# Optimization experiments

Hardware: AMD Instinct MI355X
Metric: run time of the kernel (lower is better)

Reference implementation:

```python
import jax, jax.numpy as jnp
import numpy as np

B, S, D_MODEL, H = 4, 2048, 2048, 16
HD = D_MODEL // H  # 128
ROPE_BASE = 10000.0


def apply_rope(x):
    # x: [B, H, S, HD]; interleaved-pair rotary embedding along seq axis
    s, d = x.shape[2], x.shape[3]
    inv_freq = 1.0 / (ROPE_BASE ** (jnp.arange(0, d, 2, dtype=jnp.float32) / d))  # [d/2]
    ang = jnp.arange(s, dtype=jnp.float32)[:, None] * inv_freq[None, :]  # [S, d/2]
    cos, sin = jnp.cos(ang), jnp.sin(ang)
    x0, x1 = x[..., 0::2], x[..., 1::2]  # [B,H,S,d/2]
    o0 = x0 * cos - x1 * sin
    o1 = x0 * sin + x1 * cos
    return jnp.stack([o0, o1], axis=-1).reshape(x.shape)


def setup_inputs() -> dict:
    key = jax.random.key(0)
    ks = jax.random.split(key, 5)
    sc = 1.0 / np.sqrt(D_MODEL)
    return {
        "x": jax.random.normal(ks[0], (B, S, D_MODEL), dtype=jnp.float32),
        "Wq": jax.random.normal(ks[1], (D_MODEL, D_MODEL), dtype=jnp.float32) * sc,
        "Wk": jax.random.normal(ks[2], (D_MODEL, D_MODEL), dtype=jnp.float32) * sc,
        "Wv": jax.random.normal(ks[3], (D_MODEL, D_MODEL), dtype=jnp.float32) * sc,
        "Wo": jax.random.normal(ks[4], (D_MODEL, D_MODEL), dtype=jnp.float32) * sc,
        "bo": jnp.zeros((D_MODEL,), dtype=jnp.float32),
    }


def reference(x, Wq, Wk, Wv, Wo, bo):
    b, s, _ = x.shape
    # torch Linear: y = x @ W.T (no qkv bias)
    q = (x @ Wq.T).reshape(b, s, H, HD).transpose(0, 2, 1, 3)  # [B,H,S,HD]
    k = (x @ Wk.T).reshape(b, s, H, HD).transpose(0, 2, 1, 3)
    v = (x @ Wv.T).reshape(b, s, H, HD).transpose(0, 2, 1, 3)
    q = apply_rope(q)
    k = apply_rope(k)
    scores = jnp.einsum("bhqd,bhkd->bhqk", q, k)
    causal = jnp.tril(jnp.ones((s, s), dtype=bool))
    scores = jnp.where(causal, scores, -jnp.inf)
    attn = jax.nn.softmax(scores / jnp.sqrt(jnp.float32(HD)), axis=-1)
    # dropout p=0.0 -> identity
    ctx = jnp.einsum("bhqk,bhkd->bqhd", attn, v).reshape(b, s, H * HD)
    return ctx @ Wo.T + bo
```

## Files before the change

### kernel.cpp

```cpp
#include <hip/hip_runtime.h>
#include <hip/hip_bf16.h>
#include <math.h>

#define B_  4
#define S_  2048
#define DM  2048
#define H_  16
#define HD_ 128

typedef __bf16 bf16;
typedef __bf16 bf16x4 __attribute__((ext_vector_type(4)));
typedef __bf16 bf16x8 __attribute__((ext_vector_type(8)));
typedef float  f32x4  __attribute__((ext_vector_type(4)));

__device__ __forceinline__ void gload_lds16(const bf16* g, bf16* l) {
  __builtin_amdgcn_global_load_lds(
      (const __attribute__((address_space(1))) void*)g,
      (__attribute__((address_space(3))) void*)l, 16, 0, 0);
}

__global__ void cast_f32_bf16(const float* __restrict__ src, bf16* __restrict__ dst, int n4) {
  int stride = gridDim.x * blockDim.x;
  for (int i = blockIdx.x * blockDim.x + threadIdx.x; i < n4; i += stride) {
    float4 v = reinterpret_cast<const float4*>(src)[i];
    bf16x4 o = { (bf16)v.x, (bf16)v.y, (bf16)v.z, (bf16)v.w };
    reinterpret_cast<bf16x4*>(dst)[i] = o;
  }
}

__global__ void rope_table_k(float* __restrict__ tab) {
  int idx = blockIdx.x * blockDim.x + threadIdx.x;
  if (idx >= S_ * (HD_ / 2)) return;
  int pos = idx >> 6, i = idx & 63;
  float inv = powf(10000.0f, -(2.0f * i) / (float)HD_);
  float ang = (float)pos * inv;
  tab[2 * idx]     = cosf(ang);
  tab[2 * idx + 1] = sinf(ang);
}

template<int OUTF>
__global__ __launch_bounds__(256, 2)
void gemm_bt(const bf16* __restrict__ A, const bf16* __restrict__ Bt,
             bf16* __restrict__ Cb, float* __restrict__ Cf,
             const float* __restrict__ bias, const float* __restrict__ tab,
             float scale, int M, int N, int K) {
  __shared__ bf16 As[128][32];
  __shared__ bf16 Bs[128][32];
  const int tid = threadIdx.x;
  const int w = tid >> 6, l = tid & 63;
  const int row0 = blockIdx.x * 128, col0 = blockIdx.y * 128;
  const int wm = (w >> 1) * 64, wn = (w & 1) * 64;
  const int lr = l & 15, lg = l >> 4;
  f32x4 acc[4][4] = {};
  for (int kt = 0; kt < K; kt += 32) {
    __syncthreads();
#pragma unroll
    for (int i = 0; i < 2; ++i) {
      int eo = (i * 4096 + w * 1024) / 2 + l * 8;
      int r = eo >> 5, c = eo & 31;
      gload_lds16(A  + (size_t)(row0 + r) * K + kt + c, &As[0][0] + i * 2048 + w * 512);
      gload_lds16(Bt + (size_t)(col0 + r) * K + kt + c, &Bs[0][0] + i * 2048 + w * 512);
    }
    asm volatile("s_waitcnt vmcnt(0)" ::: "memory");
    __syncthreads();
    bf16x8 af[4], bfr[4];
#pragma unroll
    for (int mi = 0; mi < 4; ++mi)
      af[mi] = *reinterpret_cast<const bf16x8*>(&As[wm + mi * 16 + lr][lg * 8]);
#pragma unroll
    for (int ni = 0; ni < 4; ++ni)
      bfr[ni] = *reinterpret_cast<const bf16x8*>(&Bs[wn + ni * 16 + lr][lg * 8]);
#pragma unroll
    for (int mi = 0; mi < 4; ++mi)
#pragma unroll
      for (int ni = 0; ni < 4; ++ni)
        acc[mi][ni] = __builtin_amdgcn_mfma_f32_16x16x32_bf16(af[mi], bfr[ni], acc[mi][ni], 0, 0, 0);
  }
#pragma unroll
  for (int mi = 0; mi < 4; ++mi) {
    int rb = row0 + wm + mi * 16 + lg * 4;
#pragma unroll
    for (int ni = 0; ni < 4; ++ni) {
      int cc = col0 + wn + ni * 16 + lr;
      if (OUTF == 2) {
        int bb = rb >> 11, s = rb & 2047;
        int hh = cc >> 7, dd = cc & 127;
        bf16x4 pack = { (bf16)acc[mi][ni][0], (bf16)acc[mi][ni][1],
                        (bf16)acc[mi][ni][2], (bf16)acc[mi][ni][3] };
        *reinterpret_cast<bf16x4*>(Cb + (((size_t)(bb * H_ + hh) * HD_ + dd) << 11) + s) = pack;
      } else if (OUTF == 3) {
        int i2 = (cc & 127) >> 1;
        float sgn = (lr & 1) ? 1.0f : -1.0f;
#pragma unroll
        for (int j = 0; j < 4; ++j) {
          float own = acc[mi][ni][j];
          float par = __shfl_xor(own, 1);
          int s = (rb + j) & (S_ - 1);
          float2 cs = reinterpret_cast<const float2*>(tab)[s * 64 + i2];
          float outv = (own * cs.x + sgn * par * cs.y) * scale;
          Cb[(size_t)(rb + j) * N + cc] = (bf16)outv;
        }
      } else {
#pragma unroll
        for (int j = 0; j < 4; ++j) {
          size_t off = (size_t)(rb + j) * N + cc;
          if (OUTF == 1) Cf[off] = acc[mi][ni][j] + bias[cc];
          else           Cb[off] = (bf16)acc[mi][ni][j];
        }
      }
    }
  }
}

__global__ __launch_bounds__(512, 4)
void attn_fwd(const bf16* __restrict__ Q, const bf16* __restrict__ K,
              const bf16* __restrict__ Vt, bf16* __restrict__ O) {
  __shared__ bf16 Ks[2][64 * 128];
  __shared__ bf16 Vs[2][128 * 64];
  __shared__ bf16 Ps[8][16 * 64];
  const int tid = threadIdx.x;
  const int w = tid >> 6, l = tid & 63;
  const int lr = l & 15, lg = l >> 4;
  const int bx = blockIdx.x;
  const int h = blockIdx.y, b = blockIdx.z;
  const size_t bbase = (size_t)b * S_ * DM + (size_t)h * HD_;
  const bf16* vtb = Vt + (size_t)(b * H_ + h) * HD_ * S_;

#pragma unroll 1
  for (int pass = 0; pass < 2; ++pass) {
    const int qt = pass ? bx : (15 - bx);
    const int q0 = qt * 128 + w * 16;
    const int ktmax = 2 * qt + 1;

    bf16x8 qf[4];
#pragma unroll
    for (int kb = 0; kb < 4; ++kb)
      qf[kb] = *reinterpret_cast<const bf16x8*>(Q + bbase + (size_t)(q0 + lr) * DM + kb * 32 + lg * 8);

    float m_r = -INFINITY;
    float l_r = 0.f;
    f32x4 o[8] = {};

#pragma unroll
    for (int i = 0; i < 2; ++i) {
      int X = w * 2048 + i * 1024 + l * 16;
      int r = X >> 8, scb = (X & 255) ^ ((r & 7) << 4);
      gload_lds16(K + bbase + (size_t)r * DM + (scb >> 1), &Ks[0][(w * 2048 + i * 1024) >> 1]);
    }
#pragma unroll
    for (int i = 0; i < 2; ++i) {
      int X = w * 2048 + i * 1024 + l * 16;
      int d = X >> 7, scb = (X & 127) ^ ((d & 7) << 4);
      gload_lds16(vtb + (size_t)d * S_ + (scb >> 1), &Vs[0][(w * 2048 + i * 1024) >> 1]);
    }

    for (int kt = 0; kt <= ktmax; ++kt) {
      const int buf = kt & 1;
      if (kt < ktmax) {
        const int nk = (kt + 1) * 64;
#pragma unroll
        for (int i = 0; i < 2; ++i) {
          int X = w * 2048 + i * 1024 + l * 16;
          int r = X >> 8, scb = (X & 255) ^ ((r & 7) << 4);
          gload_lds16(K + bbase + (size_t)(nk + r) * DM + (scb >> 1),
                      &Ks[buf ^ 1][(w * 2048 + i * 1024) >> 1]);
        }
#pragma unroll
        for (int i = 0; i < 2; ++i) {
          int X = w * 2048 + i * 1024 + l * 16;
          int d = X >> 7, scb = (X & 127) ^ ((d & 7) << 4);
          gload_lds16(vtb + (size_t)d * S_ + nk + (scb >> 1),
                      &Vs[buf ^ 1][(w * 2048 + i * 1024) >> 1]);
        }
        asm volatile("s_waitcnt vmcnt(4)" ::: "memory");
      } else {
        asm volatile("s_waitcnt vmcnt(0)" ::: "memory");
      }
      __builtin_amdgcn_s_barrier();

      f32x4 sc4[4];
      __builtin_amdgcn_s_setprio(1);
#pragma unroll
      for (int cb = 0; cb < 4; ++cb) {
        sc4[cb] = f32x4{0.f, 0.f, 0.f, 0.f};
        int r = cb * 16 + lr;
#pragma unroll
        for (int kb = 0; kb < 4; ++kb) {
          int off = r * 256 + ((kb * 64 + lg * 16) ^ ((lr & 7) << 4));
          bf16x8 kf = *reinterpret_cast<const bf16x8*>((const char*)Ks[buf] + off);
          sc4[cb] = __builtin_amdgcn_mfma_f32_16x16x32_bf16(kf, qf[kb], sc4[cb], 0, 0, 0);
        }
      }
      __builtin_amdgcn_s_setprio(0);

      const int kv0 = kt * 64;
      if (kv0 + 63 > q0) {
        const int qq = q0 + lr;
#pragma unroll
        for (int cb = 0; cb < 4; ++cb)
#pragma unroll
          for (int jj = 0; jj < 4; ++jj)
            if (kv0 + cb * 16 + lg * 4 + jj > qq) sc4[cb][jj] = -INFINITY;
      }

      float tm = -INFINITY;
#pragma unroll
      for (int cb = 0; cb < 4; ++cb)
#pragma unroll
        for (int jj = 0; jj < 4; ++jj) tm = fmaxf(tm, sc4[cb][jj]);
      tm = fmaxf(tm, __shfl_xor(tm, 16));
      tm = fmaxf(tm, __shfl_xor(tm, 32));
      float mnew = fmaxf(m_r, tm);
      float sc_f = __expf(m_r - mnew);
      m_r = mnew;
      float rs = 0.f;
#pragma unroll
      for (int cb = 0; cb < 4; ++cb)
#pragma unroll
        for (int jj = 0; jj < 4; ++jj) {
          float p = __expf(sc4[cb][jj] - mnew);
          sc4[cb][jj] = p;
          rs += p;
        }
      rs += __shfl_xor(rs, 16);
      rs += __shfl_xor(rs, 32);
      l_r = l_r * sc_f + rs;

      float scO[4];
#pragma unroll
      for (int j = 0; j < 4; ++j) scO[j] = __shfl(sc_f, lg * 4 + j);
#pragma unroll
      for (int nb = 0; nb < 8; ++nb)
#pragma unroll
        for (int j = 0; j < 4; ++j) o[nb][j] *= scO[j];

#pragma unroll
      for (int cb = 0; cb < 4; ++cb) {
        bf16x4 pk = { (bf16)sc4[cb][0], (bf16)sc4[cb][1], (bf16)sc4[cb][2], (bf16)sc4[cb][3] };
        int off = lr * 128 + ((cb * 32 + lg * 8) ^ ((lr & 7) << 4));
        *reinterpret_cast<bf16x4*>((char*)Ps[w] + off) = pk;
      }

      bf16x8 pf[2];
#pragma unroll
      for (int kc = 0; kc < 2; ++kc) {
        int off = lr * 128 + ((kc * 64 + lg * 16) ^ ((lr & 7) << 4));
        pf[kc] = *reinterpret_cast<const bf16x8*>((const char*)Ps[w] + off);
      }
      __builtin_amdgcn_s_setprio(1);
#pragma unroll
      for (int nb = 0; nb < 8; ++nb) {
        int d = nb * 16 + lr;
#pragma unroll
        for (int kc = 0; kc < 2; ++kc) {
          int off = d * 128 + ((kc * 64 + lg * 16) ^ ((lr & 7) << 4));
          bf16x8 vf = *reinterpret_cast<const bf16x8*>((const char*)Vs[buf] + off);
          o[nb] = __builtin_amdgcn_mfma_f32_16x16x32_bf16(pf[kc], vf, o[nb], 0, 0, 0);
        }
      }
      __builtin_amdgcn_s_setprio(0);

      asm volatile("s_waitcnt lgkmcnt(0)" ::: "memory");
      __builtin_amdgcn_s_barrier();
    }

    float lO[4];
#pragma unroll
    for (int j = 0; j < 4; ++j) lO[j] = __shfl(l_r, lg * 4 + j);
#pragma unroll
    for (int j = 0; j < 4; ++j) {
      float inv = 1.0f / lO[j];
      size_t rowoff = bbase + (size_t)(q0 + lg * 4 + j) * DM;
#pragma unroll
      for (int nb = 0; nb < 8; ++nb)
        O[rowoff + nb * 16 + lr] = (bf16)(o[nb][j] * inv);
    }
  }
}

extern "C" void kernel_launch(void* const* d_in, const int* in_sizes, int n_in,
                              void* d_out, int out_size, void* d_ws, size_t ws_size,
                              hipStream_t stream) {
  const float* x  = (const float*)d_in[0];
  const float* Wq = (const float*)d_in[1];
  const float* Wk = (const float*)d_in[2];
  const float* Wv = (const float*)d_in[3];
  const float* Wo = (const float*)d_in[4];
  const float* bo = (const float*)d_in[5];
  float* out = (float*)d_out;

  const size_t NX = (size_t)B_ * S_ * DM;
  const size_t NW = (size_t)DM * DM;
  char* ws = (char*)d_ws;
  bf16* xb   = (bf16*)ws; ws += NX * 2;
  bf16* wqb  = (bf16*)ws; ws += NW * 2;
  bf16* wkb  = (bf16*)ws; ws += NW * 2;
  bf16* wvb  = (bf16*)ws; ws += NW * 2;
  bf16* wob  = (bf16*)ws; ws += NW * 2;
  bf16* qb   = (bf16*)ws; ws += NX * 2;
  bf16* kb   = (bf16*)ws; ws += NX * 2;
  bf16* vt   = (bf16*)ws; ws += NX * 2;
  bf16* ctxb = (bf16*)ws; ws += NX * 2;
  float* tab = (float*)ws; ws += (size_t)S_ * 64 * 2 * sizeof(float);

  cast_f32_bf16<<<(int)((NX / 4 + 255) / 256), 256, 0, stream>>>(x, xb, (int)(NX / 4));
  cast_f32_bf16<<<(int)((NW / 4 + 255) / 256), 256, 0, stream>>>(Wq, wqb, (int)(NW / 4));
  cast_f32_bf16<<<(int)((NW / 4 + 255) / 256), 256, 0, stream>>>(Wk, wkb, (int)(NW / 4));
  cast_f32_bf16<<<(int)((NW / 4 + 255) / 256), 256, 0, stream>>>(Wv, wvb, (int)(NW / 4));
  cast_f32_bf16<<<(int)((NW / 4 + 255) / 256), 256, 0, stream>>>(Wo, wob, (int)(NW / 4));
  rope_table_k<<<(S_ * 64 + 255) / 256, 256, 0, stream>>>(tab);

  const int M = B_ * S_;
  dim3 gg(M / 128, DM / 128);
  gemm_bt<3><<<gg, 256, 0, stream>>>(xb, wqb, qb, nullptr, nullptr, tab, 0.08838834764831845f, M, DM, DM);
  gemm_bt<3><<<gg, 256, 0, stream>>>(xb, wkb, kb, nullptr, nullptr, tab, 1.0f, M, DM, DM);
  gemm_bt<2><<<gg, 256, 0, stream>>>(xb, wvb, vt, nullptr, nullptr, nullptr, 0.f, M, DM, DM);

  attn_fwd<<<dim3(8, H_, B_), 512, 0, stream>>>(qb, kb, vt, ctxb);

  gemm_bt<1><<<gg, 256, 0, stream>>>(ctxb, wob, nullptr, out, bo, nullptr, 0.f, M, DM, DM);
}
```

Baseline: 487.1 us.

## Fuse QKV projections into one 512x128-tile GEMM with triple-buffered swizzled LDS

Replaces the 128x128 single-buffered GEMM with a 512-thread kernel that computes 512x128 tiles. Global-to-LDS loads run through a three-stage ring buffer with partial vmcnt waits, and the LDS layout is XOR-swizzled to avoid bank conflicts. The Q, K and V weights are concatenated so a single launch produces all three projections, with the epilogue choosing RoPE or the transposed V store by column region. The aim is more operand reuse per tile, loads overlapped with MFMA work, and fewer launches. The cost is higher register and LDS use (about 120KB LDS), which lowers occupancy.

```diff
diff --git a/kernel.cpp b/kernel.cpp
--- a/kernel.cpp
+++ b/kernel.cpp
@@ -38,74 +38,116 @@
   tab[2 * idx + 1] = sinf(ang);
 }
 
-template<int OUTF>
-__global__ __launch_bounds__(256, 2)
-void gemm_bt(const bf16* __restrict__ A, const bf16* __restrict__ Bt,
-             bf16* __restrict__ Cb, float* __restrict__ Cf,
-             const float* __restrict__ bias, const float* __restrict__ tab,
-             float scale, int M, int N, int K) {
-  __shared__ bf16 As[128][32];
-  __shared__ bf16 Bs[128][32];
+template<int EPI>
+__global__ __launch_bounds__(512, 2)
+void gemm512(const bf16* __restrict__ A, const bf16* __restrict__ Bt,
+             bf16* __restrict__ Oq, bf16* __restrict__ Ok, bf16* __restrict__ Ovt,
+             float* __restrict__ Cf, const float* __restrict__ bias,
+             const float* __restrict__ tab, int N, int K) {
+  __shared__ bf16 lds[61440];
   const int tid = threadIdx.x;
   const int w = tid >> 6, l = tid & 63;
-  const int row0 = blockIdx.x * 128, col0 = blockIdx.y * 128;
-  const int wm = (w >> 1) * 64, wn = (w & 1) * 64;
   const int lr = l & 15, lg = l >> 4;
-  f32x4 acc[4][4] = {};
-  for (int kt = 0; kt < K; kt += 32) {
-    __syncthreads();
-#pragma unroll
-    for (int i = 0; i < 2; ++i) {
-      int eo = (i * 4096 + w * 1024) / 2 + l * 8;
-      int r = eo >> 5, c = eo & 31;
-      gload_lds16(A  + (size_t)(row0 + r) * K + kt + c, &As[0][0] + i * 2048 + w * 512);
-      gload_lds16(Bt + (size_t)(col0 + r) * K + kt + c, &Bs[0][0] + i * 2048 + w * 512);
-    }
-    asm volatile("s_waitcnt vmcnt(0)" ::: "memory");
-    __syncthreads();
-    bf16x8 af[4], bfr[4];
-#pragma unroll
-    for (int mi = 0; mi < 4; ++mi)
-      af[mi] = *reinterpret_cast<const bf16x8*>(&As[wm + mi * 16 + lr][lg * 8]);
-#pragma unroll
-    for (int ni = 0; ni < 4; ++ni)
-      bfr[ni] = *reinterpret_cast<const bf16x8*>(&Bs[wn + ni * 16 + lr][lg * 8]);
-#pragma unroll
-    for (int mi = 0; mi < 4; ++mi)
+  const int row0 = blockIdx.y * 512, col0 = blockIdx.x * 128;
+  const int wm = w >> 1, wn = w & 1;
+  const int NT = K / 32;
+
+  auto stage = [&](int t, int c) {
+    const bf16* Ab = A + (size_t)row0 * K + t * 32;
+    const bf16* Bb = Bt + (size_t)col0 * K + t * 32;
+    bf16* base = lds + c * 20480;
+#pragma unroll
+    for (int i = 0; i < 4; ++i) {
+      int D = w * 4096 + i * 1024 + l * 16;
+      int r = D >> 6;
+      int gk = ((D & 63) ^ (((r >> 1) & 3) << 4)) >> 1;
+      gload_lds16(Ab + (size_t)r * K + gk, base + ((w * 4096 + i * 1024) >> 1));
+    }
+    {
+      int D = w * 1024 + l * 16;
+      int r = D >> 6;
+      int gk = ((D & 63) ^ (((r >> 1) & 3) << 4)) >> 1;
+      gload_lds16(Bb + (size_t)r * K + gk, base + 16384 + ((w * 1024) >> 1));
+    }
+  };
+
+  int offA[8], offB[4];
+#pragma unroll
+  for (int mi = 0; mi < 8; ++mi) {
+    int r = wm * 128 + mi * 16 + lr;
+    offA[mi] = r * 64 + ((lg * 16) ^ (((r >> 1) & 3) << 4));
+  }
+#pragma unroll
+  for (int ni = 0; ni < 4; ++ni) {
+    int r = wn * 64 + ni * 16 + lr;
+    offB[ni] = 32768 + r * 64 + ((lg * 16) ^ (((r >> 1) & 3) << 4));
+  }
+
+  f32x4 acc[8][4] = {};
+  stage(0, 0);
+  stage(1, 1);
+
+  for (int t = 0; t < NT; ++t) {
+    const int c = t % 3;
+    if (t + 2 < NT) {
+      stage(t + 2, (t + 2) % 3);
+      asm volatile("s_waitcnt vmcnt(10)" ::: "memory");
+    } else if (t + 1 < NT) {
+      asm volatile("s_waitcnt vmcnt(5)" ::: "memory");
+    } else {
+      asm volatile("s_waitcnt vmcnt(0)" ::: "memory");
+    }
+    __builtin_amdgcn_s_barrier();
+
+    const char* bb = (const char*)lds + c * 40960;
+    bf16x8 af[8], bfr[4];
+#pragma unroll
+    for (int mi = 0; mi < 8; ++mi) af[mi] = *reinterpret_cast<const bf16x8*>(bb + offA[mi]);
+#pragma unroll
+    for (int ni = 0; ni < 4; ++ni) bfr[ni] = *reinterpret_cast<const bf16x8*>(bb + offB[ni]);
+
+    __builtin_amdgcn_s_setprio(1);
+#pragma unroll
+    for (int mi = 0; mi < 8; ++mi)
 #pragma unroll
       for (int ni = 0; ni < 4; ++ni)
         acc[mi][ni] = __builtin_amdgcn_mfma_f32_16x16x32_bf16(af[mi], bfr[ni], acc[mi][ni], 0, 0, 0);
-  }
-#pragma unroll
-  for (int mi = 0; mi < 4; ++mi) {
-    int rb = row0 + wm + mi * 16 + lg * 4;
+    __builtin_amdgcn_s_setprio(0);
+    __builtin_amdgcn_s_barrier();
+  }
+
+#pragma unroll
+  for (int mi = 0; mi < 8; ++mi) {
+    int rb = row0 + wm * 128 + mi * 16 + lg * 4;
 #pragma unroll
     for (int ni = 0; ni < 4; ++ni) {
-      int cc = col0 + wn + ni * 16 + lr;
-      if (OUTF == 2) {
-        int bb = rb >> 11, s = rb & 2047;
-        int hh = cc >> 7, dd = cc & 127;
-        bf16x4 pack = { (bf16)acc[mi][ni][0], (bf16)acc[mi][ni][1],
-                        (bf16)acc[mi][ni][2], (bf16)acc[mi][ni][3] };
-        *reinterpret_cast<bf16x4*>(Cb + (((size_t)(bb * H_ + hh) * HD_ + dd) << 11) + s) = pack;
-      } else if (OUTF == 3) {
-        int i2 = (cc & 127) >> 1;
-        float sgn = (lr & 1) ? 1.0f : -1.0f;
-#pragma unroll
-        for (int j = 0; j < 4; ++j) {
-          float own = acc[mi][ni][j];
-          float par = __shfl_xor(own, 1);
-          int s = (rb + j) & (S_ - 1);
-          float2 cs = reinterpret_cast<const float2*>(tab)[s * 64 + i2];
-          float outv = (own * cs.x + sgn * par * cs.y) * scale;
-          Cb[(size_t)(rb + j) * N + cc] = (bf16)outv;
-        }
+      int gc = col0 + wn * 64 + ni * 16 + lr;
+      if (EPI == 1) {
+#pragma unroll
+        for (int j = 0; j < 4; ++j)
+          Cf[(size_t)(rb + j) * N + gc] = acc[mi][ni][j] + bias[gc];
       } else {
-#pragma unroll
-        for (int j = 0; j < 4; ++j) {
-          size_t off = (size_t)(rb + j) * N + cc;
-          if (OUTF == 1) Cf[off] = acc[mi][ni][j] + bias[cc];
-          else           Cb[off] = (bf16)acc[mi][ni][j];
+        int reg = col0 >> 11;
+        int cc = gc & 2047;
+        if (reg == 2) {
+          int bb2 = rb >> 11, s = rb & 2047;
+          int hh = cc >> 7, dd = cc & 127;
+          bf16x4 pack = { (bf16)acc[mi][ni][0], (bf16)acc[mi][ni][1],
+                          (bf16)acc[mi][ni][2], (bf16)acc[mi][ni][3] };
+          *reinterpret_cast<bf16x4*>(Ovt + (((size_t)(bb2 * H_ + hh) * HD_ + dd) << 11) + s) = pack;
+        } else {
+          bf16* Dst = (reg == 0) ? Oq : Ok;
+          float scale = (reg == 0) ? 0.08838834764831845f : 1.0f;
+          int i2 = (cc & 127) >> 1;
+          float sgn = (lr & 1) ? 1.0f : -1.0f;
+#pragma unroll
+          for (int j = 0; j < 4; ++j) {
+            float own = acc[mi][ni][j];
+            float par = __shfl_xor(own, 1);
+            int s = (rb + j) & (S_ - 1);
+            float2 cs = reinterpret_cast<const float2*>(tab)[s * 64 + i2];
+            Dst[(size_t)(rb + j) * 2048 + cc] = (bf16)((own * cs.x + sgn * par * cs.y) * scale);
+          }
         }
       }
     }
@@ -293,9 +335,7 @@
   const size_t NW = (size_t)DM * DM;
   char* ws = (char*)d_ws;
   bf16* xb   = (bf16*)ws; ws += NX * 2;
-  bf16* wqb  = (bf16*)ws; ws += NW * 2;
-  bf16* wkb  = (bf16*)ws; ws += NW * 2;
-  bf16* wvb  = (bf16*)ws; ws += NW * 2;
+  bf16* wqkv = (bf16*)ws; ws += 3 * NW * 2;
   bf16* wob  = (bf16*)ws; ws += NW * 2;
   bf16* qb   = (bf16*)ws; ws += NX * 2;
   bf16* kb   = (bf16*)ws; ws += NX * 2;
@@ -304,19 +344,18 @@
   float* tab = (float*)ws; ws += (size_t)S_ * 64 * 2 * sizeof(float);
 
   cast_f32_bf16<<<(int)((NX / 4 + 255) / 256), 256, 0, stream>>>(x, xb, (int)(NX / 4));
-  cast_f32_bf16<<<(int)((NW / 4 + 255) / 256), 256, 0, stream>>>(Wq, wqb, (int)(NW / 4));
-  cast_f32_bf16<<<(int)((NW / 4 + 255) / 256), 256, 0, stream>>>(Wk, wkb, (int)(NW / 4));
-  cast_f32_bf16<<<(int)((NW / 4 + 255) / 256), 256, 0, stream>>>(Wv, wvb, (int)(NW / 4));
+  cast_f32_bf16<<<(int)((NW / 4 + 255) / 256), 256, 0, stream>>>(Wq, wqkv, (int)(NW / 4));
+  cast_f32_bf16<<<(int)((NW / 4 + 255) / 256), 256, 0, stream>>>(Wk, wqkv + NW, (int)(NW / 4));
+  cast_f32_bf16<<<(int)((NW / 4 + 255) / 256), 256, 0, stream>>>(Wv, wqkv + 2 * NW, (int)(NW / 4));
   cast_f32_bf16<<<(int)((NW / 4 + 255) / 256), 256, 0, stream>>>(Wo, wob, (int)(NW / 4));
   rope_table_k<<<(S_ * 64 + 255) / 256, 256, 0, stream>>>(tab);
 
   const int M = B_ * S_;
-  dim3 gg(M / 128, DM / 128);
-  gemm_bt<3><<<gg, 256, 0, stream>>>(xb, wqb, qb, nullptr, nullptr, tab, 0.08838834764831845f, M, DM, DM);
-  gemm_bt<3><<<gg, 256, 0, stream>>>(xb, wkb, kb, nullptr, nullptr, tab, 1.0f, M, DM, DM);
-  gemm_bt<2><<<gg, 256, 0, stream>>>(xb, wvb, vt, nullptr, nullptr, nullptr, 0.f, M, DM, DM);
+  gemm512<0><<<dim3(3 * DM / 128, M / 512), 512, 0, stream>>>(
+      xb, wqkv, qb, kb, vt, nullptr, nullptr, tab, 3 * DM, DM);
 
   attn_fwd<<<dim3(8, H_, B_), 512, 0, stream>>>(qb, kb, vt, ctxb);
 
-  gemm_bt<1><<<gg, 256, 0, stream>>>(ctxb, wob, nullptr, out, bo, nullptr, 0.f, M, DM, DM);
-}
+  gemm512<1><<<dim3(DM / 128, M / 512), 512, 0, stream>>>(
+      ctxb, wob, nullptr, nullptr, nullptr, out, bo, nullptr, DM, DM);
+}
```

Result: faster. 472.6 us (-3.0%).
